# Kernel tuning notes

Measured on AMD Instinct MI355X. Metric: run time of the kernel, lower is better.

The kernel has to match this reference:

```python
import jax, jax.numpy as jnp
import numpy as np

THRESHOLD = 0.5
MARGIN = 0.5
MIN_PIXELS = 64


def make_grid(h, w):
    # Faithful to SpatialClustering.make_grid
    if w >= h:
        xm = jnp.broadcast_to(jnp.linspace(0.0, w / h, w).reshape(1, 1, w), (1, h, w))
        ym = jnp.broadcast_to(jnp.linspace(0.0, 1.0, h).reshape(1, h, 1), (1, h, w))
    else:
        xm = jnp.broadcast_to(jnp.linspace(0.0, 1.0, w).reshape(1, 1, w), (1, h, w))
        ym = jnp.broadcast_to(jnp.linspace(0.0, h / w, h).reshape(1, h, 1), (1, h, w))
    return jnp.concatenate([xm, ym], axis=0)  # (2, h, w)


def cluster_per_image(x, grid_flat):
    # x: (5, h, w); grid_flat: (2, N)
    c, h, w = x.shape
    N = h * w
    offset = x[0:2].reshape(2, N)
    sigma = x[2:4].reshape(2, N)
    seed_raw = x[4].reshape(N)

    spa_emb = jnp.tanh(offset) + grid_flat          # (2, N)
    seed_map = jax.nn.sigmoid(seed_raw)             # (N,)
    valid = seed_raw > THRESHOLD                    # (N,) == torch `mask`

    # In torch: masked_select restricts to `valid` pixels; here we keep the
    # full N-length arrays and carry `valid`/`unclustered` boolean masks.
    # unclustered starts as `valid`, so the torch outer guard
    # (mask.sum() > min_pixels) coincides with the first while-cond check.

    def cond(state):
        unclustered, inst, count, done = state
        return (jnp.sum(unclustered) > MIN_PIXELS) & jnp.logical_not(done)

    def body(state):
        unclustered, inst, count, done = state
        score = jnp.where(unclustered, seed_map, 0.0)
        idx = jnp.argmax(score)
        sc = score[idx]
        new_done = sc < THRESHOLD  # torch `break` -> revert this iteration's updates

        uncl2 = unclustered.at[idx].set(False)  # torch: unclustered[seed] = 0 before ratio
        center = spa_emb[:, idx]                # (2,)
        s = sigma[:, idx]                       # (2,)
        # exp(-sum((e-c)^2 / (2 s^2)))
        dist = jnp.exp(-jnp.sum((spa_emb - center[:, None]) ** 2 / (2.0 * s[:, None] ** 2), axis=0))  # (N,)
        proposal = (dist > MARGIN) & valid

        pc = jnp.sum(proposal)
        uc = jnp.sum(proposal & uncl2)
        # torch: proposal.sum() > min_pixels  and  unclustered[proposal].sum()/proposal.sum() > 0.5
        accept = (pc > MIN_PIXELS) & (2 * uc > pc)

        inst_new = jnp.where(accept & proposal, count, inst)
        count_new = count + accept.astype(jnp.int32)
        uncl_new = uncl2 & jnp.logical_not(proposal)  # torch: unclustered[proposal] = 0

        unclustered = jnp.where(new_done, unclustered, uncl_new)
        inst = jnp.where(new_done, inst, inst_new)
        count = jnp.where(new_done, count, count_new)
        return (unclustered, inst, count, new_done)

    init = (valid, jnp.zeros(N, dtype=jnp.int32), jnp.int32(1), jnp.array(False))
    _, inst, _, _ = jax.lax.while_loop(cond, body, init)
    return inst.reshape(h, w)


def setup_inputs() -> dict:
    key = jax.random.key(0)
    k1, k2, k3 = jax.random.split(key, 3)
    B, H, W = 4, 512, 1024
    offset = jax.random.normal(k1, (B, 2, H, W), dtype=jnp.float32)
    # sigma in [0.2, 0.45]: realistic per-pixel bandwidths so exp-distance
    # proposals cover cluster-sized regions and the greedy loop terminates.
    sigma = jax.random.uniform(k2, (B, 2, H, W), dtype=jnp.float32, minval=0.2, maxval=0.45)
    seed = jax.random.normal(k3, (B, 1, H, W), dtype=jnp.float32)
    tag_pred = jnp.concatenate([offset, sigma, seed], axis=1)  # (B, 5, H, W)
    return {"tag_pred": tag_pred}


def reference(tag_pred):
    b, c, h, w = tag_pred.shape
    grid_flat = make_grid(h, w).reshape(2, h * w)
    f = lambda x: cluster_per_image(x, grid_flat)
    inst = jax.lax.map(f, tag_pred)  # sequential per-image greedy clustering
    return inst.astype(jnp.uint8)    # (b, h, w) instance map, ids 0 = background
```

## Files before the change

### kernel.cpp

```cpp
#include <hip/hip_runtime.h>
#include <math.h>

#define BATCH 4
#define HH 512
#define WW 1024
#define NPIX (HH*WW)
#define CCAP 196608
#define GX 64
#define GY 48
#define NCELL (GX*GY)
#define CELL 0.0625f
#define INVCELL 16.0f
#define SEGSZ 256
#define NSEGMAX (CCAP/SEGSZ)
#define DLCAP 2048
#define CKCAP 1600

__device__ __forceinline__ float xla_tanhf(float x) {
  if (fabsf(x) < 0.0004f) return x;
  float xc = fminf(fmaxf(x, -7.90531110763549805f), 7.90531110763549805f);
  float x2 = __fmul_rn(xc, xc);
  float p = -2.76076847742355e-16f;
  p = fmaf(x2, p, 2.00018790482477e-13f);
  p = fmaf(x2, p, -8.60467152213735e-11f);
  p = fmaf(x2, p, 5.12229709037114e-08f);
  p = fmaf(x2, p, 1.48572235717979e-05f);
  p = fmaf(x2, p, 6.37261928875436e-04f);
  p = fmaf(x2, p, 4.89352455891786e-03f);
  p = __fmul_rn(xc, p);
  float q = fmaf(x2, 1.19825839466702e-06f, 1.18534705686654e-04f);
  q = fmaf(x2, q, 2.26843463243900e-03f);
  q = fmaf(x2, q, 4.89352518554385e-03f);
  return __fdiv_rn(p, q);
}

__device__ __forceinline__ float xla_expf(float x) {
  float xc = fminf(fmaxf(x, -87.3365478515625f), 88.72283935546875f);
  float m = floorf(fmaf(xc, 1.44269504088896341f, 0.5f));
  float r = fmaf(m, -0.693359375f, xc);
  r = fmaf(m, 2.12194440e-4f, r);
  float r2 = __fmul_rn(r, r);
  float p = 1.9875691500e-4f;
  p = fmaf(p, r, 1.3981999507e-3f);
  p = fmaf(p, r, 8.3334519073e-3f);
  p = fmaf(p, r, 4.1665795894e-2f);
  p = fmaf(p, r, 1.6666665459e-1f);
  p = fmaf(p, r, 5.0000001201e-1f);
  float y = fmaf(r2, p, r);
  y = __fadd_rn(y, 1.0f);
  return ldexpf(y, (int)m);
}

__device__ __forceinline__ float xla_sigmoidf(float x) {
  return fmaf(0.5f, xla_tanhf(__fmul_rn(0.5f, x)), 0.5f);
}

__device__ __forceinline__ bool prop_test(float2 e, float cx, float cy,
                                          float den0, float den1,
                                          float inv0, float inv1) {
  float d0 = __fsub_rn(e.x, cx), d1 = __fsub_rn(e.y, cy);
  float dd0 = __fmul_rn(d0, d0), dd1 = __fmul_rn(d1, d1);
  float zf = fmaf(dd0, inv0, __fmul_rn(dd1, inv1));
  if (zf < 0.6921472f) return true;
  if (zf <= 0.6941472f) {
    float t0 = __fdiv_rn(dd0, den0);
    float t1 = __fdiv_rn(dd1, den1);
    float z = __fadd_rn(t0, t1);
    return xla_expf(-z) > 0.5f;
  }
  return false;
}

__device__ __forceinline__ int cell_of_x(float ex) {
  int c = (int)((ex + 1.0f) * INVCELL);
  return min(max(c, 0), GX - 1);
}
__device__ __forceinline__ int cell_of_y(float ey) {
  int c = (int)((ey + 1.0f) * INVCELL);
  return min(max(c, 0), GY - 1);
}


__global__ __launch_bounds__(1024) void fill_kernel(int* out, int val, int n) {
  int i = blockIdx.x * 1024 + threadIdx.x;
  if (i < n) out[i] = val;
}

__global__ __launch_bounds__(1024) void hist_kernel(const float* __restrict__ in,
                                                    int* __restrict__ out,
                                                    int* __restrict__ hist) {
  __shared__ int lh[NCELL];
  int tid = threadIdx.x;
  int gid = blockIdx.x * 1024 + tid;
  int b = gid >> 19;
  int p = gid & (NPIX - 1);
  for (int j = tid; j < NCELL; j += 1024) lh[j] = 0;
  __syncthreads();
  const float* base = in + (size_t)b * 5 * NPIX;
  float seed = base[(size_t)4 * NPIX + p];
  out[gid] = 0;
  if (seed > 0.5f) {
    float ox = base[p];
    float oy = base[(size_t)NPIX + p];
    int col = p & (WW - 1);
    int row = p >> 10;
    float gx = __fmul_rn((float)col, 2.0f / 1023.0f);
    float gy = __fmul_rn((float)row, 1.0f / 511.0f);
    float ex = __fadd_rn(xla_tanhf(ox), gx);
    float ey = __fadd_rn(xla_tanhf(oy), gy);
    atomicAdd(&lh[cell_of_y(ey) * GX + cell_of_x(ex)], 1);
  }
  __syncthreads();
  for (int j = tid; j < NCELL; j += 1024) {
    int c = lh[j];
    if (c) atomicAdd(&hist[b * NCELL + j], c);
  }
}

__global__ __launch_bounds__(1024) void scan_kernel(const int* __restrict__ hist,
                                                    int* __restrict__ off,
                                                    int* __restrict__ cursor) {
  __shared__ int s_c[NCELL];
  __shared__ int s_ps[1024];
  int b = blockIdx.x, t = threadIdx.x;
  const int* h = hist + b * NCELL;
  for (int i = t; i < NCELL; i += 1024) s_c[i] = h[i];
  __syncthreads();
  int a = s_c[3 * t], b2 = s_c[3 * t + 1], c2 = s_c[3 * t + 2];
  int th = a + b2 + c2;
  s_ps[t] = th;
  __syncthreads();
  for (int d = 1; d < 1024; d <<= 1) {
    int v = (t >= d) ? s_ps[t - d] : 0;
    __syncthreads();
    s_ps[t] += v;
    __syncthreads();
  }
  int excl = s_ps[t] - th;
  int* ob = off + b * (NCELL + 1);
  int* cb = cursor + b * NCELL;
  ob[3 * t] = excl;              cb[3 * t] = excl;
  ob[3 * t + 1] = excl + a;      cb[3 * t + 1] = excl + a;
  ob[3 * t + 2] = excl + a + b2; cb[3 * t + 2] = excl + a + b2;
  if (t == 1023) ob[NCELL] = s_ps[1023];
}

__global__ __launch_bounds__(1024) void scatter_kernel(const float* __restrict__ in,
                                                       int* __restrict__ cursor,
                                                       float2* __restrict__ emb,
                                                       int2* __restrict__ pk) {
  __shared__ int lh[NCELL];
  __shared__ int lbase[NCELL];
  int tid = threadIdx.x;
  int gid = blockIdx.x * 1024 + tid;
  int b = gid >> 19;
  int p = gid & (NPIX - 1);
  for (int j = tid; j < NCELL; j += 1024) lh[j] = 0;
  __syncthreads();
  const float* base = in + (size_t)b * 5 * NPIX;
  float seed = base[(size_t)4 * NPIX + p];
  bool valid = seed > 0.5f;
  float ex = 0.0f, ey = 0.0f, smv = 0.0f;
  int cell = 0, sl = 0;
  if (valid) {
    float ox = base[p];
    float oy = base[(size_t)NPIX + p];
    int col = p & (WW - 1);
    int row = p >> 10;
    float gx = __fmul_rn((float)col, 2.0f / 1023.0f);
    float gy = __fmul_rn((float)row, 1.0f / 511.0f);
    ex = __fadd_rn(xla_tanhf(ox), gx);
    ey = __fadd_rn(xla_tanhf(oy), gy);
    smv = xla_sigmoidf(seed);
    cell = cell_of_y(ey) * GX + cell_of_x(ex);
    sl = atomicAdd(&lh[cell], 1);
  }
  __syncthreads();
  for (int j = tid; j < NCELL; j += 1024) {
    int c = lh[j];
    if (c) lbase[j] = atomicAdd(&cursor[b * NCELL + j], c);
  }
  __syncthreads();
  if (valid) {
    int slot = lbase[cell] + sl;
    if (slot < CCAP) {
      emb[(size_t)b * CCAP + slot] = make_float2(ex, ey);
      pk[(size_t)b * CCAP + slot]  = make_int2(__float_as_int(smv), p);
    }
  }
}

__device__ __forceinline__ void seg_rescan(int s, int V, int lane,
    const unsigned* s_uncl, const int2* __restrict__ pk,
    const float2* __restrict__ emb, const float* __restrict__ base,
    unsigned long long* s_segkey, int* s_segci, float4* s_segaux,
    bool checkAlive) {
  unsigned long long bk = 0ULL; int bci = -1; int bpx = 0;
  #pragma unroll
  for (int j = 0; j < 4; ++j) {
    int i = (s << 8) + (j << 6) + lane;
    if (i < V) {
      bool alive = !checkAlive || ((s_uncl[i >> 5] >> (i & 31)) & 1u);
      if (alive) {
        int2 v = pk[i];
        unsigned long long k = ((unsigned long long)(unsigned)v.x << 32) | (unsigned)(~v.y);
        if (k > bk) { bk = k; bci = i; bpx = v.y; }
      }
    }
  }
  unsigned long long mk = bk; int mci = bci;
  #pragma unroll
  for (int o = 1; o < 64; o <<= 1) {
    unsigned long long ok = __shfl_xor(mk, o);
    int oci = __shfl_xor(mci, o);
    if (ok > mk) { mk = ok; mci = oci; }
  }
  if (lane == 0) { s_segkey[s] = mk; s_segci[s] = mci; }
  if (mk != 0ULL && bk == mk) {
    float2 e = emb[mci];
    float sxv = base[(size_t)2 * NPIX + bpx];
    float syv = base[(size_t)3 * NPIX + bpx];
    float d0 = __fmul_rn(2.0f, __fmul_rn(sxv, sxv));
    float d1 = __fmul_rn(2.0f, __fmul_rn(syv, syv));
    s_segaux[s] = make_float4(e.x, e.y, d0, d1);
  }
}

__global__ __launch_bounds__(1024) void cluster_kernel(const float* __restrict__ in,
                                                       int* __restrict__ out,
                                                       const float2* __restrict__ emb_all,
                                                       const int2* __restrict__ pk_all,
                                                       const int* __restrict__ off_g) {
  __shared__ unsigned int s_uncl[CCAP / 32];
  __shared__ int s_off[NCELL + 1];
  __shared__ unsigned long long s_segkey[NSEGMAX];
  __shared__ int s_segci[NSEGMAX];
  __shared__ float4 s_segaux[NSEGMAX];
  __shared__ int s_dlist[DLCAP];
  __shared__ int s_ck[CKCAP];
  __shared__ int4 s_row4[24];
  __shared__ int s_pc[2];
  __shared__ int s_uc[2];
  __shared__ int s_nd[2];

  int b = blockIdx.x;
  int tid = threadIdx.x;
  int lane = tid & 63;
  int wid = tid >> 6;
  const int* offb = off_g + b * (NCELL + 1);
  int V = offb[NCELL];
  const float2* emb = emb_all + (size_t)b * CCAP;
  const int2*   pk  = pk_all  + (size_t)b * CCAP;
  int* outb = out + (size_t)b * NPIX;
  const float* base = in + (size_t)b * 5 * NPIX;

  if (V > CCAP) {
    for (int i = tid; i < NPIX; i += 1024) outb[i] = 1000000;
    return;
  }
  int NSEG = (V + SEGSZ - 1) >> 8;

  for (int i = tid; i <= NCELL; i += 1024) s_off[i] = offb[i];
  for (int w = tid; w < CCAP / 32; w += 1024) {
    int basebit = w << 5;
    unsigned m;
    if (basebit + 32 <= V)      m = 0xffffffffu;
    else if (basebit >= V)      m = 0u;
    else                        m = (1u << (V - basebit)) - 1u;
    s_uncl[w] = m;
  }
  if (tid < 2) { s_pc[tid] = 0; s_uc[tid] = 0; s_nd[tid] = 0; }
  __syncthreads();

  for (int s = wid; s < NSEG; s += 16)
    seg_rescan(s, V, lane, s_uncl, pk, emb, base, s_segkey, s_segci, s_segaux, false);
  __syncthreads();

  int ucount = V, count = 1, guard = 0;
  int t = 0;
  while (ucount > 64 && guard++ <= CCAP) {
    int cur = t & 1, nxt = cur ^ 1;

    unsigned long long lk = 0ULL; int lsg = -1;
    for (int s = lane; s < NSEG; s += 64) {
      unsigned long long v = s_segkey[s];
      if (v > lk) { lk = v; lsg = s; }
    }
    unsigned long long gk = lk;
    #pragma unroll
    for (int o = 1; o < 64; o <<= 1) {
      unsigned long long ok = __shfl_xor(gk, o);
      if (ok > gk) gk = ok;
    }
    if (gk == 0ULL) break;
    float sm = __uint_as_float((unsigned)(gk >> 32));
    if (sm < 0.5f) break;
    unsigned long long bmask = __ballot(lk == gk);
    int src = __builtin_ctzll(bmask);
    int sg = __shfl(lsg, src);

    float4 aux = s_segaux[sg];
    float cx = aux.x, cy = aux.y, den0 = aux.z, den1 = aux.w;
    float inv0 = 1.0f / den0;
    float inv1 = 1.0f / den1;
    float ry = sqrtf(__fmul_rn(den1, 0.6971472f)) * 1.00001f;
    int r0 = cell_of_y(cy - ry);
    int r1 = cell_of_y(cy + ry);
    int nr = r1 - r0 + 1;

    int ck = 0, rs_l = 0, re_l = 0, m0_l = 0, m1_l = 0;
    if (lane < nr) {
      int r = r0 + lane;
      float ylo = fmaf((float)r, CELL, -1.0f);
      float dy = fmaxf(0.0f, fmaxf(ylo - cy, cy - (ylo + CELL))) * 0.999999f;
      float rem = 0.6971472f - dy * dy * inv1;
      if (rem > 0.0f) {
        float dxm = sqrtf(den0 * rem) * 1.00001f;
        int c0 = cell_of_x(cx - dxm), c1 = cell_of_x(cx + dxm);
        int rbase = r * GX;
        rs_l = s_off[rbase + c0]; re_l = s_off[rbase + c1 + 1];
        m0_l = rs_l; m1_l = rs_l;
        float dyc = fmaxf(fabsf(ylo - cy), fabsf(ylo + CELL - cy)) + 1e-5f;
        float remI = 0.6920f - dyc * dyc * inv1;
        if (remI > 0.0f) {
          float dxin = sqrtf(den0 * remI) * 0.9999f;
          int a  = (int)ceilf(fmaf(cx - dxin, INVCELL, INVCELL) + 1e-3f);
          int bb = (int)floorf(fmaf(cx + dxin, INVCELL, INVCELL) - 1e-3f) - 1;
          a = max(a, c0); bb = min(bb, c1);
          if (a <= bb) { m0_l = s_off[rbase + a]; m1_l = s_off[rbase + bb + 1]; }
        }
        ck = (re_l - rs_l + 127) >> 7;
      }
    }
    int cum = ck;
    #pragma unroll
    for (int o = 1; o < 32; o <<= 1) {
      int u = __shfl_up(cum, o);
      if (lane >= o) cum += u;
    }
    int nc = __shfl(cum, 31);
    int excl = cum - ck;
    if (lane < nr && ck) {
      s_row4[lane] = make_int4(m0_l, m1_l, re_l, 0);
      for (int k = 0; k < ck; ++k)
        s_ck[excl + k] = (lane << 24) | (rs_l + (k << 7));
    }

    int pc = 0, uc = 0;
    for (int c = wid; c < nc; c += 16) {
      int e = s_ck[c];
      int rl = e >> 24;
      int i0 = e & 0xffffff;
      int4 rw = s_row4[rl];
      int hi = min(i0 + 128, rw.z);
      int i = i0 + lane, i2 = i + 64;
      bool p0, p1;
      if (i0 >= rw.x && i0 + 128 <= rw.y) {
        p0 = i < hi; p1 = i2 < hi;
      } else {
        p0 = (i < hi) && ((i >= rw.x && i < rw.y) ||
                          prop_test(emb[i], cx, cy, den0, den1, inv0, inv1));
        p1 = (i2 < hi) && ((i2 >= rw.x && i2 < rw.y) ||
                           prop_test(emb[i2], cx, cy, den0, den1, inv0, inv1));
      }
      unsigned long long bm0 = __ballot(p0);
      unsigned long long bm1 = __ballot(p1);
      if ((bm0 | bm1) == 0ULL) continue;
      int off = i0 & 31;
      unsigned w = (unsigned)(i0 >> 5);
      unsigned bits = 0; unsigned tw = w;
      if (lane == 0)      { pc += (int)__popcll(bm0); bits = (unsigned)(bm0 << off); tw = w; }
      else if (lane == 1) { bits = (unsigned)(bm0 >> (32 - off)); tw = w + 1; }
      else if (lane == 2) { if (off > 0) bits = (unsigned)(bm0 >> (64 - off)); tw = w + 2; }
      else if (lane == 3) { pc += (int)__popcll(bm1); bits = (unsigned)(bm1 << off); tw = w + 2; }
      else if (lane == 4) { bits = (unsigned)(bm1 >> (32 - off)); tw = w + 3; }
      else if (lane == 5) { if (off > 0) bits = (unsigned)(bm1 >> (64 - off)); tw = w + 4; }
      if (bits) {
        unsigned old = atomicAnd(&s_uncl[tw], ~bits);
        unsigned remv = old & bits;
        if (remv) {
          uc += __popc(remv);
          int seg = (int)(tw >> 3);
          int ciw = s_segci[seg];
          if ((ciw >> 5) == (int)tw && ((remv >> (ciw & 31)) & 1u)) {
            int pos = atomicAdd(&s_nd[cur], 1);
            if (pos < DLCAP) s_dlist[pos] = seg;
          }
        }
      }
    }
    for (int o = 32; o > 0; o >>= 1) {
      pc += __shfl_down(pc, o);
      uc += __shfl_down(uc, o);
    }
    if (lane == 0 && (pc | uc)) {
      if (pc) atomicAdd(&s_pc[cur], pc);
      if (uc) atomicAdd(&s_uc[cur], uc);
    }
    __syncthreads();

    int pcT = s_pc[cur];
    int ucR = s_uc[cur];
    int ndRaw = s_nd[cur];
    bool accept = (pcT > 64) && (2 * (ucR - 1) > pcT);
    int label = count & 255;
    if (accept) count++;
    ucount -= ucR;
    if (tid == 0) { s_pc[nxt] = 0; s_uc[nxt] = 0; s_nd[nxt] = 0; }

    if (accept) {
      for (int c = wid; c < nc; c += 16) {
        int e = s_ck[c];
        int rl = e >> 24;
        int i0 = e & 0xffffff;
        int4 rw = s_row4[rl];
        int hi = min(i0 + 128, rw.z);
        int i = i0 + lane, i2 = i + 64;
        if (i < hi && ((i >= rw.x && i < rw.y) ||
                       prop_test(emb[i], cx, cy, den0, den1, inv0, inv1)))
          outb[pk[i].y] = label;
        if (i2 < hi && ((i2 >= rw.x && i2 < rw.y) ||
                        prop_test(emb[i2], cx, cy, den0, den1, inv0, inv1)))
          outb[pk[i2].y] = label;
      }
    }

    if (ndRaw > DLCAP) {
      for (int s = wid; s < NSEG; s += 16)
        seg_rescan(s, V, lane, s_uncl, pk, emb, base, s_segkey, s_segci, s_segaux, true);
    } else {
      for (int d = wid; d < ndRaw; d += 16)
        seg_rescan(s_dlist[d], V, lane, s_uncl, pk, emb, base, s_segkey, s_segci, s_segaux, true);
    }
    __syncthreads();
    t++;
  }
}


extern "C" void kernel_launch(void* const* d_in, const int* in_sizes, int n_in,
                              void* d_out, int out_size, void* d_ws, size_t ws_size,
                              hipStream_t stream) {
  const float* in = (const float*)d_in[0];
  int* out = (int*)d_out;

  size_t hist_bytes = (size_t)BATCH * NCELL * sizeof(int);
  size_t off_bytes  = (size_t)BATCH * (NCELL + 1) * sizeof(int);
  size_t cur_bytes  = (size_t)BATCH * NCELL * sizeof(int);
  size_t emb_bytes  = (size_t)BATCH * CCAP * sizeof(float2);
  size_t pk_bytes   = (size_t)BATCH * CCAP * sizeof(int2);

  size_t o_hist = 256;
  size_t o_off  = (o_hist + hist_bytes + 255) & ~(size_t)255;
  size_t o_cur  = (o_off + off_bytes + 255) & ~(size_t)255;
  size_t o_emb  = (o_cur + cur_bytes + 255) & ~(size_t)255;
  size_t o_pk   = (o_emb + emb_bytes + 255) & ~(size_t)255;
  size_t need   = o_pk + pk_bytes;

  if (ws_size < need) {
    fill_kernel<<<(out_size + 1023) / 1024, 1024, 0, stream>>>(out, 2000000, out_size);
    return;
  }

  int*    hist = (int*)((char*)d_ws + o_hist);
  int*    off  = (int*)((char*)d_ws + o_off);
  int*    cur  = (int*)((char*)d_ws + o_cur);
  float2* emb  = (float2*)((char*)d_ws + o_emb);
  int2*   pk   = (int2*)((char*)d_ws + o_pk);

  hipMemsetAsync(hist, 0, hist_bytes, stream);
  hist_kernel<<<(BATCH * NPIX) / 1024, 1024, 0, stream>>>(in, out, hist);
  scan_kernel<<<BATCH, 1024, 0, stream>>>(hist, off, cur);
  scatter_kernel<<<(BATCH * NPIX) / 1024, 1024, 0, stream>>>(in, cur, emb, pk);
  cluster_kernel<<<BATCH, 1024, 0, stream>>>(in, out, emb, pk, off);
}
```

Before: 945.2 us.

## Speculatively process two spatially disjoint seeds per greedy clustering iteration

Each segment now tracks its second-best key. The global reduction finds the top two seeds, and when their proposal bounding ellipses cannot overlap, both clusters are evaluated in the same iteration. This roughly halves the number of serialized block-wide iterations, each of which needs syncs. The chunk list becomes an int4 per chunk carrying the candidate id and the row bounds, and the DLCAP/CKCAP sizes are reduced to make room in shared memory. The risk is subtle divergence from the sequential greedy semantics, for example when seed B's alive status depends on A's removal; the check on the segment's second key is meant to guard this. The added reduction and selection work also costs something every iteration.

```diff
diff --git a/kernel.cpp b/kernel.cpp
--- a/kernel.cpp
+++ b/kernel.cpp
@@ -13,8 +13,8 @@
 #define INVCELL 16.0f
 #define SEGSZ 256
 #define NSEGMAX (CCAP/SEGSZ)
-#define DLCAP 2048
-#define CKCAP 1600
+#define DLCAP 1024
+#define CKCAP 1024
 
 __device__ __forceinline__ float xla_tanhf(float x) {
   if (fabsf(x) < 0.0004f) return x;
@@ -193,9 +193,9 @@
 __device__ __forceinline__ void seg_rescan(int s, int V, int lane,
     const unsigned* s_uncl, const int2* __restrict__ pk,
     const float2* __restrict__ emb, const float* __restrict__ base,
-    unsigned long long* s_segkey, int* s_segci, float4* s_segaux,
-    bool checkAlive) {
-  unsigned long long bk = 0ULL; int bci = -1; int bpx = 0;
+    unsigned long long* s_segkey, unsigned long long* s_segkey2,
+    int* s_segci, float4* s_segaux, bool checkAlive) {
+  unsigned long long bk = 0ULL, bk2 = 0ULL; int bci = -1; int bpx = 0;
   #pragma unroll
   for (int j = 0; j < 4; ++j) {
     int i = (s << 8) + (j << 6) + lane;
@@ -204,18 +204,23 @@
       if (alive) {
         int2 v = pk[i];
         unsigned long long k = ((unsigned long long)(unsigned)v.x << 32) | (unsigned)(~v.y);
-        if (k > bk) { bk = k; bci = i; bpx = v.y; }
-      }
-    }
-  }
-  unsigned long long mk = bk; int mci = bci;
+        if (k > bk) { bk2 = bk; bk = k; bci = i; bpx = v.y; }
+        else if (k > bk2) bk2 = k;
+      }
+    }
+  }
+  unsigned long long mk = bk, mk2 = bk2; int mci = bci;
   #pragma unroll
   for (int o = 1; o < 64; o <<= 1) {
     unsigned long long ok = __shfl_xor(mk, o);
+    unsigned long long ok2 = __shfl_xor(mk2, o);
     int oci = __shfl_xor(mci, o);
+    unsigned long long lo = (mk < ok) ? mk : ok;
+    unsigned long long hi2 = (mk2 > ok2) ? mk2 : ok2;
     if (ok > mk) { mk = ok; mci = oci; }
-  }
-  if (lane == 0) { s_segkey[s] = mk; s_segci[s] = mci; }
+    mk2 = (lo > hi2) ? lo : hi2;
+  }
+  if (lane == 0) { s_segkey[s] = mk; s_segkey2[s] = mk2; s_segci[s] = mci; }
   if (mk != 0ULL && bk == mk) {
     float2 e = emb[mci];
     float sxv = base[(size_t)2 * NPIX + bpx];
@@ -234,13 +239,13 @@
   __shared__ unsigned int s_uncl[CCAP / 32];
   __shared__ int s_off[NCELL + 1];
   __shared__ unsigned long long s_segkey[NSEGMAX];
+  __shared__ unsigned long long s_segkey2[NSEGMAX];
   __shared__ int s_segci[NSEGMAX];
   __shared__ float4 s_segaux[NSEGMAX];
   __shared__ int s_dlist[DLCAP];
-  __shared__ int s_ck[CKCAP];
-  __shared__ int4 s_row4[24];
-  __shared__ int s_pc[2];
-  __shared__ int s_uc[2];
+  __shared__ int4 s_ck4[CKCAP];
+  __shared__ int s_pc[2][2];
+  __shared__ int s_uc[2][2];
   __shared__ int s_nd[2];
 
   int b = blockIdx.x;
@@ -269,11 +274,12 @@
     else                        m = (1u << (V - basebit)) - 1u;
     s_uncl[w] = m;
   }
-  if (tid < 2) { s_pc[tid] = 0; s_uc[tid] = 0; s_nd[tid] = 0; }
+  if (tid < 2) { s_pc[tid][0] = 0; s_pc[tid][1] = 0; s_uc[tid][0] = 0; s_uc[tid][1] = 0; s_nd[tid] = 0; }
   __syncthreads();
 
   for (int s = wid; s < NSEG; s += 16)
-    seg_rescan(s, V, lane, s_uncl, pk, emb, base, s_segkey, s_segci, s_segaux, false);
+    seg_rescan(s, V, lane, s_uncl, pk, emb, base, s_segkey, s_segkey2,
+               s_segci, s_segaux, false);
   __syncthreads();
 
   int ucount = V, count = 1, guard = 0;
@@ -281,87 +287,131 @@
   while (ucount > 64 && guard++ <= CCAP) {
     int cur = t & 1, nxt = cur ^ 1;
 
-    unsigned long long lk = 0ULL; int lsg = -1;
+    unsigned long long lk = 0ULL, lk2 = 0ULL; int lsg = -1, lsg2 = -1;
     for (int s = lane; s < NSEG; s += 64) {
       unsigned long long v = s_segkey[s];
-      if (v > lk) { lk = v; lsg = s; }
-    }
-    unsigned long long gk = lk;
+      if (v > lk) { lk2 = lk; lsg2 = lsg; lk = v; lsg = s; }
+      else if (v > lk2) { lk2 = v; lsg2 = s; }
+    }
+    unsigned long long gk = lk, gk2 = lk2; int gsg = lsg, gsg2 = lsg2;
     #pragma unroll
     for (int o = 1; o < 64; o <<= 1) {
       unsigned long long ok = __shfl_xor(gk, o);
-      if (ok > gk) gk = ok;
+      unsigned long long ok2 = __shfl_xor(gk2, o);
+      int osg = __shfl_xor(gsg, o);
+      int osg2 = __shfl_xor(gsg2, o);
+      if (ok > gk) {
+        unsigned long long c = gk; int csg = gsg;
+        gk = ok; gsg = osg;
+        if (c >= ok2) { gk2 = c; gsg2 = csg; } else { gk2 = ok2; gsg2 = osg2; }
+      } else if (ok > gk2) { gk2 = ok; gsg2 = osg; }
     }
     if (gk == 0ULL) break;
     float sm = __uint_as_float((unsigned)(gk >> 32));
     if (sm < 0.5f) break;
-    unsigned long long bmask = __ballot(lk == gk);
-    int src = __builtin_ctzll(bmask);
-    int sg = __shfl(lsg, src);
-
-    float4 aux = s_segaux[sg];
-    float cx = aux.x, cy = aux.y, den0 = aux.z, den1 = aux.w;
-    float inv0 = 1.0f / den0;
-    float inv1 = 1.0f / den1;
-    float ry = sqrtf(__fmul_rn(den1, 0.6971472f)) * 1.00001f;
-    int r0 = cell_of_y(cy - ry);
-    int r1 = cell_of_y(cy + ry);
-    int nr = r1 - r0 + 1;
-
-    int ck = 0, rs_l = 0, re_l = 0, m0_l = 0, m1_l = 0;
-    if (lane < nr) {
-      int r = r0 + lane;
+
+    float4 auxA = s_segaux[gsg];
+    float cxA = auxA.x, cyA = auxA.y, den0A = auxA.z, den1A = auxA.w;
+    float inv0A = 1.0f / den0A, inv1A = 1.0f / den1A;
+    float rxA = sqrtf(__fmul_rn(den0A, 0.6971472f)) * 1.00001f;
+    float ryA = sqrtf(__fmul_rn(den1A, 0.6971472f)) * 1.00001f;
+    int r0A = cell_of_y(cyA - ryA), r1A = cell_of_y(cyA + ryA);
+    int nrA = r1A - r0A + 1;
+
+    bool spec0 = false;
+    float cxB = 0, cyB = 0, den0B = 1, den1B = 1, inv0B = 1, inv1B = 1;
+    int r0B = 0, nrB = 0;
+    if (gk2 != 0ULL) {
+      float sm2 = __uint_as_float((unsigned)(gk2 >> 32));
+      if (sm2 >= 0.5f && s_segkey2[gsg] < gk2) {
+        float4 auxB = s_segaux[gsg2];
+        cxB = auxB.x; cyB = auxB.y; den0B = auxB.z; den1B = auxB.w;
+        float rxB = sqrtf(__fmul_rn(den0B, 0.6971472f)) * 1.00001f;
+        float ryB = sqrtf(__fmul_rn(den1B, 0.6971472f)) * 1.00001f;
+        if (fabsf(cxA - cxB) > rxA + rxB + 1e-3f ||
+            fabsf(cyA - cyB) > ryA + ryB + 1e-3f) {
+          spec0 = true;
+          inv0B = 1.0f / den0B; inv1B = 1.0f / den1B;
+          int r1B = cell_of_y(cyB + ryB);
+          r0B = cell_of_y(cyB - ryB);
+          nrB = r1B - r0B + 1;
+        }
+      }
+    }
+
+    int candl = lane >> 5;
+    int rr = lane & 31;
+    int nrc = candl ? (spec0 ? nrB : 0) : nrA;
+    int ckl = 0, rsl = 0, rel = 0, m0l = 0, m1l = 0;
+    if (rr < nrc) {
+      int r = (candl ? r0B : r0A) + rr;
+      float CY = candl ? cyB : cyA;
+      float CX = candl ? cxB : cxA;
+      float D0 = candl ? den0B : den0A;
+      float I1 = candl ? inv1B : inv1A;
       float ylo = fmaf((float)r, CELL, -1.0f);
-      float dy = fmaxf(0.0f, fmaxf(ylo - cy, cy - (ylo + CELL))) * 0.999999f;
-      float rem = 0.6971472f - dy * dy * inv1;
+      float dy = fmaxf(0.0f, fmaxf(ylo - CY, CY - (ylo + CELL))) * 0.999999f;
+      float rem = 0.6971472f - dy * dy * I1;
       if (rem > 0.0f) {
-        float dxm = sqrtf(den0 * rem) * 1.00001f;
-        int c0 = cell_of_x(cx - dxm), c1 = cell_of_x(cx + dxm);
+        float dxm = sqrtf(D0 * rem) * 1.00001f;
+        int c0 = cell_of_x(CX - dxm), c1 = cell_of_x(CX + dxm);
         int rbase = r * GX;
-        rs_l = s_off[rbase + c0]; re_l = s_off[rbase + c1 + 1];
-        m0_l = rs_l; m1_l = rs_l;
-        float dyc = fmaxf(fabsf(ylo - cy), fabsf(ylo + CELL - cy)) + 1e-5f;
-        float remI = 0.6920f - dyc * dyc * inv1;
+        rsl = s_off[rbase + c0]; rel = s_off[rbase + c1 + 1];
+        m0l = rsl; m1l = rsl;
+        float dyc = fmaxf(fabsf(ylo - CY), fabsf(ylo + CELL - CY)) + 1e-5f;
+        float remI = 0.6920f - dyc * dyc * I1;
         if (remI > 0.0f) {
-          float dxin = sqrtf(den0 * remI) * 0.9999f;
-          int a  = (int)ceilf(fmaf(cx - dxin, INVCELL, INVCELL) + 1e-3f);
-          int bb = (int)floorf(fmaf(cx + dxin, INVCELL, INVCELL) - 1e-3f) - 1;
+          float dxin = sqrtf(D0 * remI) * 0.9999f;
+          int a  = (int)ceilf(fmaf(CX - dxin, INVCELL, INVCELL) + 1e-3f);
+          int bb = (int)floorf(fmaf(CX + dxin, INVCELL, INVCELL) - 1e-3f) - 1;
           a = max(a, c0); bb = min(bb, c1);
-          if (a <= bb) { m0_l = s_off[rbase + a]; m1_l = s_off[rbase + bb + 1]; }
+          if (a <= bb) { m0l = s_off[rbase + a]; m1l = s_off[rbase + bb + 1]; }
         }
-        ck = (re_l - rs_l + 127) >> 7;
-      }
-    }
-    int cum = ck;
+        ckl = (rel - rsl + 127) >> 7;
+      }
+    }
+    int pxl = (candl == 0) ? (rel - rsl) : 0;
     #pragma unroll
-    for (int o = 1; o < 32; o <<= 1) {
+    for (int o = 1; o < 64; o <<= 1) pxl += __shfl_xor(pxl, o);
+    bool dual = spec0 && (ucount > 64 + pxl);
+    if (!dual && candl) ckl = 0;
+
+    int cum = ckl;
+    #pragma unroll
+    for (int o = 1; o < 64; o <<= 1) {
       int u = __shfl_up(cum, o);
       if (lane >= o) cum += u;
     }
-    int nc = __shfl(cum, 31);
-    int excl = cum - ck;
-    if (lane < nr && ck) {
-      s_row4[lane] = make_int4(m0_l, m1_l, re_l, 0);
-      for (int k = 0; k < ck; ++k)
-        s_ck[excl + k] = (lane << 24) | (rs_l + (k << 7));
-    }
-
-    int pc = 0, uc = 0;
+    int nc = __shfl(cum, 63);
+    int excl = cum - ckl;
+    for (int k = 0; k < ckl; ++k) {
+      int pos = excl + k;
+      if ((pos & 15) == wid) {
+        int i0 = rsl + (k << 7);
+        s_ck4[pos] = make_int4(i0 | (candl << 24), min(i0 + 128, rel), m0l, m1l);
+      }
+    }
+
+    int pcL0 = 0, ucL0 = 0, pcL1 = 0, ucL1 = 0;
     for (int c = wid; c < nc; c += 16) {
-      int e = s_ck[c];
-      int rl = e >> 24;
-      int i0 = e & 0xffffff;
-      int4 rw = s_row4[rl];
-      int hi = min(i0 + 128, rw.z);
+      int4 e = s_ck4[c];
+      int cand = e.x >> 24;
+      int i0 = e.x & 0xffffff;
+      int hi = e.y, M0 = e.z, M1 = e.w;
+      float CX = cand ? cxB : cxA;
+      float CY = cand ? cyB : cyA;
+      float D0 = cand ? den0B : den0A;
+      float D1 = cand ? den1B : den1A;
+      float I0 = cand ? inv0B : inv0A;
+      float I1 = cand ? inv1B : inv1A;
       int i = i0 + lane, i2 = i + 64;
       bool p0, p1;
-      if (i0 >= rw.x && i0 + 128 <= rw.y) {
-        p0 = i < hi; p1 = i2 < hi;
-      } else {
-        p0 = (i < hi) && ((i >= rw.x && i < rw.y) ||
-                          prop_test(emb[i], cx, cy, den0, den1, inv0, inv1));
-        p1 = (i2 < hi) && ((i2 >= rw.x && i2 < rw.y) ||
-                           prop_test(emb[i2], cx, cy, den0, den1, inv0, inv1));
+      if (i0 >= M0 && i0 + 128 <= M1) { p0 = i < hi; p1 = i2 < hi; }
+      else {
+        p0 = (i < hi) && ((i >= M0 && i < M1) ||
+                          prop_test(emb[i], CX, CY, D0, D1, I0, I1));
+        p1 = (i2 < hi) && ((i2 >= M0 && i2 < M1) ||
+                           prop_test(emb[i2], CX, CY, D0, D1, I0, I1));
       }
       unsigned long long bm0 = __ballot(p0);
       unsigned long long bm1 = __ballot(p1);
@@ -369,17 +419,20 @@
       int off = i0 & 31;
       unsigned w = (unsigned)(i0 >> 5);
       unsigned bits = 0; unsigned tw = w;
-      if (lane == 0)      { pc += (int)__popcll(bm0); bits = (unsigned)(bm0 << off); tw = w; }
+      if (lane == 0)      { int x = (int)__popcll(bm0); if (cand) pcL1 += x; else pcL0 += x;
+                            bits = (unsigned)(bm0 << off); tw = w; }
       else if (lane == 1) { bits = (unsigned)(bm0 >> (32 - off)); tw = w + 1; }
       else if (lane == 2) { if (off > 0) bits = (unsigned)(bm0 >> (64 - off)); tw = w + 2; }
-      else if (lane == 3) { pc += (int)__popcll(bm1); bits = (unsigned)(bm1 << off); tw = w + 2; }
+      else if (lane == 3) { int x = (int)__popcll(bm1); if (cand) pcL1 += x; else pcL0 += x;
+                            bits = (unsigned)(bm1 << off); tw = w + 2; }
       else if (lane == 4) { bits = (unsigned)(bm1 >> (32 - off)); tw = w + 3; }
       else if (lane == 5) { if (off > 0) bits = (unsigned)(bm1 >> (64 - off)); tw = w + 4; }
       if (bits) {
         unsigned old = atomicAnd(&s_uncl[tw], ~bits);
         unsigned remv = old & bits;
         if (remv) {
-          uc += __popc(remv);
+          int x = __popc(remv);
+          if (cand) ucL1 += x; else ucL0 += x;
           int seg = (int)(tw >> 3);
           int ciw = s_segci[seg];
           if ((ciw >> 5) == (int)tw && ((remv >> (ciw & 31)) & 1u)) {
@@ -389,48 +442,69 @@
         }
       }
     }
+    #pragma unroll
     for (int o = 32; o > 0; o >>= 1) {
-      pc += __shfl_down(pc, o);
-      uc += __shfl_down(uc, o);
-    }
-    if (lane == 0 && (pc | uc)) {
-      if (pc) atomicAdd(&s_pc[cur], pc);
-      if (uc) atomicAdd(&s_uc[cur], uc);
+      pcL0 += __shfl_down(pcL0, o); ucL0 += __shfl_down(ucL0, o);
+      pcL1 += __shfl_down(pcL1, o); ucL1 += __shfl_down(ucL1, o);
+    }
+    if (lane == 0) {
+      if (pcL0) atomicAdd(&s_pc[cur][0], pcL0);
+      if (ucL0) atomicAdd(&s_uc[cur][0], ucL0);
+      if (pcL1) atomicAdd(&s_pc[cur][1], pcL1);
+      if (ucL1) atomicAdd(&s_uc[cur][1], ucL1);
     }
     __syncthreads();
 
-    int pcT = s_pc[cur];
-    int ucR = s_uc[cur];
+    int pcTA = s_pc[cur][0], ucA = s_uc[cur][0];
     int ndRaw = s_nd[cur];
-    bool accept = (pcT > 64) && (2 * (ucR - 1) > pcT);
-    int label = count & 255;
-    if (accept) count++;
-    ucount -= ucR;
-    if (tid == 0) { s_pc[nxt] = 0; s_uc[nxt] = 0; s_nd[nxt] = 0; }
-
-    if (accept) {
+    bool acceptA = (pcTA > 64) && (2 * (ucA - 1) > pcTA);
+    int labelA = count & 255;
+    if (acceptA) count++;
+    int removed = ucA;
+    bool acceptB = false; int labelB = 0;
+    if (dual) {
+      int pcTB = s_pc[cur][1], ucB = s_uc[cur][1];
+      acceptB = (pcTB > 64) && (2 * (ucB - 1) > pcTB);
+      labelB = count & 255;
+      if (acceptB) count++;
+      removed += ucB;
+    }
+    ucount -= removed;
+    if (tid == 0) { s_pc[nxt][0] = 0; s_pc[nxt][1] = 0;
+                    s_uc[nxt][0] = 0; s_uc[nxt][1] = 0; s_nd[nxt] = 0; }
+
+    if (acceptA || acceptB) {
       for (int c = wid; c < nc; c += 16) {
-        int e = s_ck[c];
-        int rl = e >> 24;
-        int i0 = e & 0xffffff;
-        int4 rw = s_row4[rl];
-        int hi = min(i0 + 128, rw.z);
+        int4 e = s_ck4[c];
+        int cand = e.x >> 24;
+        if (cand ? !acceptB : !acceptA) continue;
+        int label = cand ? labelB : labelA;
+        int i0 = e.x & 0xffffff;
+        int hi = e.y, M0 = e.z, M1 = e.w;
+        float CX = cand ? cxB : cxA;
+        float CY = cand ? cyB : cyA;
+        float D0 = cand ? den0B : den0A;
+        float D1 = cand ? den1B : den1A;
+        float I0 = cand ? inv0B : inv0A;
+        float I1 = cand ? inv1B : inv1A;
         int i = i0 + lane, i2 = i + 64;
-        if (i < hi && ((i >= rw.x && i < rw.y) ||
-                       prop_test(emb[i], cx, cy, den0, den1, inv0, inv1)))
+        if (i < hi && ((i >= M0 && i < M1) ||
+                       prop_test(emb[i], CX, CY, D0, D1, I0, I1)))
           outb[pk[i].y] = label;
-        if (i2 < hi && ((i2 >= rw.x && i2 < rw.y) ||
-                        prop_test(emb[i2], cx, cy, den0, den1, inv0, inv1)))
+        if (i2 < hi && ((i2 >= M0 && i2 < M1) ||
+                        prop_test(emb[i2], CX, CY, D0, D1, I0, I1)))
           outb[pk[i2].y] = label;
       }
     }
 
     if (ndRaw > DLCAP) {
       for (int s = wid; s < NSEG; s += 16)
-        seg_rescan(s, V, lane, s_uncl, pk, emb, base, s_segkey, s_segci, s_segaux, true);
+        seg_rescan(s, V, lane, s_uncl, pk, emb, base, s_segkey, s_segkey2,
+                   s_segci, s_segaux, true);
     } else {
       for (int d = wid; d < ndRaw; d += 16)
-        seg_rescan(s_dlist[d], V, lane, s_uncl, pk, emb, base, s_segkey, s_segci, s_segaux, true);
+        seg_rescan(s_dlist[d], V, lane, s_uncl, pk, emb, base, s_segkey,
+                   s_segkey2, s_segci, s_segaux, true);
     }
     __syncthreads();
     t++;
```

Measured after the change: 989.9 us. 1.05x slower.
